# Performance work log

Hardware: AMD Instinct MI355X
Metric: run time of the kernel (lower is better)

Reference implementation:

```python
import math
import jax, jax.numpy as jnp
import numpy as np

B, S, D = 2, 2048, 1024
N_HEADS, D_KV = 16, 64
INNER = N_HEADS * D_KV
NUM_BUCKETS = 32
MAX_DISTANCE = 128


def _relative_position_bucket(relative_position, num_buckets=NUM_BUCKETS, max_distance=MAX_DISTANCE):
    # bidirectional (encoder) variant
    nb = num_buckets // 2
    rel_buckets = (relative_position > 0).astype(jnp.int32) * nb
    rp = jnp.abs(relative_position)
    max_exact = nb // 2
    is_small = rp < max_exact
    rp_safe = jnp.maximum(rp, 1)  # avoid log(0); selected away by where
    rp_if_large = max_exact + (
        jnp.log(rp_safe.astype(jnp.float32) / max_exact)
        / math.log(max_distance / max_exact)
        * (nb - max_exact)
    ).astype(jnp.int32)
    rp_if_large = jnp.minimum(rp_if_large, nb - 1)
    return rel_buckets + jnp.where(is_small, rp, rp_if_large)


def compute_bias(rel_bias, q_len, k_len):
    ctx = jnp.arange(q_len)[:, None]
    mem = jnp.arange(k_len)[None, :]
    buckets = _relative_position_bucket(mem - ctx)  # [q_len, k_len]
    values = rel_bias[buckets]                      # [q_len, k_len, H]
    return jnp.transpose(values, (2, 0, 1))[None]   # [1, H, q_len, k_len]


def setup_inputs() -> dict:
    key = jax.random.key(0)
    ks = jax.random.split(key, 6)
    s = 1.0 / math.sqrt(D)
    return {
        "hidden_states": jax.random.normal(ks[0], (B, S, D), jnp.float32),
        "wq": jax.random.normal(ks[1], (D, INNER), jnp.float32) * s,
        "wk": jax.random.normal(ks[2], (D, INNER), jnp.float32) * s,
        "wv": jax.random.normal(ks[3], (D, INNER), jnp.float32) * s,
        "wo": jax.random.normal(ks[4], (INNER, D), jnp.float32) * s,
        "rel_bias": jax.random.normal(ks[5], (NUM_BUCKETS, N_HEADS), jnp.float32) * 0.1,
    }


def reference(hidden_states, wq, wk, wv, wo, rel_bias):
    b, s, _ = hidden_states.shape

    def shape(x):  # [b, s, inner] -> [b, h, s, d_kv]
        return x.reshape(b, s, N_HEADS, D_KV).transpose(0, 2, 1, 3)

    q = shape(hidden_states @ wq)  # note: T5 has NO 1/sqrt(d) scaling
    k = shape(hidden_states @ wk)
    v = shape(hidden_states @ wv)

    scores = jnp.einsum("bhqd,bhkd->bhqk", q, k)
    position_bias = compute_bias(rel_bias, s, s)
    scores = scores + position_bias
    attn = jax.nn.softmax(scores.astype(jnp.float32), axis=-1).astype(scores.dtype)

    out = jnp.einsum("bhqk,bhkd->bhqd", attn, v)
    out = out.transpose(0, 2, 1, 3).reshape(b, s, INNER)
    return out @ wo
```

## Files before the change

### kernel.cpp

```cpp
#include <hip/hip_runtime.h>
#include <hip/hip_bf16.h>

#define B_ 2
#define S_ 2048
#define D_ 1024
#define H_ 16
#define DKV_ 64
#define INNER_ 1024
#define M_ (B_*S_)

typedef unsigned short ushort_t;
typedef unsigned int u32;
typedef __bf16 bf16x8 __attribute__((ext_vector_type(8)));
typedef __bf16 bf16x4 __attribute__((ext_vector_type(4)));
typedef float f32x4 __attribute__((ext_vector_type(4)));

#define VMCNT0 asm volatile("s_waitcnt vmcnt(0)" ::: "memory")
#define VMCNT4 asm volatile("s_waitcnt vmcnt(4)" ::: "memory")
#define LOG2E 1.4426950408889634f

__device__ __forceinline__ unsigned short f2bf(float f) {
    unsigned int u = __builtin_bit_cast(unsigned int, f);
    unsigned int r = (u + 0x7fffu + ((u >> 16) & 1u)) >> 16;
    return (unsigned short)r;
}

__device__ __forceinline__ void gload16(const ushort_t* g, ushort_t* l) {
    __builtin_amdgcn_global_load_lds(
        (const __attribute__((address_space(1))) u32*)g,
        (__attribute__((address_space(3))) u32*)l, 16, 0, 0);
}

__global__ __launch_bounds__(256) void cvt_bf16(const float* __restrict__ in,
                                                unsigned short* __restrict__ out, int n) {
    int i = (blockIdx.x * 256 + threadIdx.x) * 4;
    if (i < n) {
        float4 v = *(const float4*)&in[i];
        ushort4 o;
        o.x = f2bf(v.x); o.y = f2bf(v.y); o.z = f2bf(v.z); o.w = f2bf(v.w);
        *(ushort4*)&out[i] = o;
    }
}

__global__ __launch_bounds__(256) void transp_bf16(
        const float* __restrict__ s0, const float* __restrict__ s1,
        const float* __restrict__ s2, const float* __restrict__ s3,
        unsigned short* __restrict__ d0, unsigned short* __restrict__ d1,
        unsigned short* __restrict__ d2, unsigned short* __restrict__ d3) {
    const float* srcs[4] = {s0, s1, s2, s3};
    unsigned short* dsts[4] = {d0, d1, d2, d3};
    const float* src = srcs[blockIdx.z];
    unsigned short* dst = dsts[blockIdx.z];
    __shared__ float t[64][65];
    int k0 = blockIdx.y * 64, n0 = blockIdx.x * 64;
    for (int i = threadIdx.x; i < 4096; i += 256) {
        int r = i >> 6, c = i & 63;
        t[r][c] = src[(k0 + r) * 1024 + n0 + c];
    }
    __syncthreads();
    for (int i = threadIdx.x; i < 4096; i += 256) {
        int r = i >> 6, c = i & 63;
        dst[(n0 + r) * 1024 + k0 + c] = f2bf(t[c][r]);
    }
}

__global__ __launch_bounds__(256) void bias_kernel(const float* __restrict__ rb,
                                                   float* __restrict__ btab) {
    int idx = blockIdx.x * 256 + threadIdx.x;
    int h = idx >> 12, pos = idx & 4095;
    int rel = pos - 2048;
    int bb = rel > 0 ? 16 : 0;
    int rp = rel < 0 ? -rel : rel;
    int bucket;
    if (rp < 8) bucket = bb + rp;
    else {
        int v = 8 + (int)(logf((float)rp * 0.125f) / 2.7725887f * 8.0f);
        bucket = bb + (v < 15 ? v : 15);
    }
    btab[idx] = rb[bucket * 16 + h] * LOG2E;
}

__global__ __launch_bounds__(256) void gemm_qkv(const ushort_t* __restrict__ A,
        const ushort_t* __restrict__ WQ, const ushort_t* __restrict__ WK, const ushort_t* __restrict__ WV,
        ushort_t* __restrict__ Qb, ushort_t* __restrict__ Kb, ushort_t* __restrict__ Vtb) {
    __shared__ alignas(16) ushort_t As[128][64];
    __shared__ alignas(16) ushort_t Bs[128][64];
    int tid = threadIdx.x, wid = tid >> 6, lane = tid & 63;
    int linear = blockIdx.x;
    int swz = (linear & 7) * 96 + (linear >> 3);
    int m0 = (swz / 24) * 128;
    int nblk = swz % 24;
    int sel = nblk >> 3;
    const ushort_t* Bt = sel == 0 ? WQ : (sel == 1 ? WK : WV);
    int n0 = (nblk & 7) * 128;
    int lr = lane & 15, lg = lane >> 4;
    int wm = (wid >> 1) * 64, wn = (wid & 1) * 64;
    int srow = tid >> 3, sp = tid & 7;
    int scol = (sp ^ (srow & 7)) * 8;
    int cR0 = (lg ^ (lr & 7)) * 8;
    int cR1 = ((4 + lg) ^ (lr & 7)) * 8;
    const ushort_t* Abase = A + (size_t)m0 * 1024 + scol;
    const ushort_t* Bbase = Bt + (size_t)n0 * 1024 + scol;
    f32x4 acc[4][4] = {};
    for (int kt = 0; kt < 1024; kt += 64) {
        #pragma unroll
        for (int j = 0; j < 4; ++j) {
            int row = j * 32 + srow;
            gload16(Abase + row * 1024 + kt, &As[0][0] + (j * 256 + tid) * 8);
            gload16(Bbase + row * 1024 + kt, &Bs[0][0] + (j * 256 + tid) * 8);
        }
        VMCNT0;
        __syncthreads();
        bf16x8 af[4][2], bfr[4][2];
        #pragma unroll
        for (int t = 0; t < 4; ++t) {
            af[t][0]  = *(const bf16x8*)&As[wm + t * 16 + lr][cR0];
            af[t][1]  = *(const bf16x8*)&As[wm + t * 16 + lr][cR1];
            bfr[t][0] = *(const bf16x8*)&Bs[wn + t * 16 + lr][cR0];
            bfr[t][1] = *(const bf16x8*)&Bs[wn + t * 16 + lr][cR1];
        }
        #pragma unroll
        for (int hh = 0; hh < 2; ++hh)
            #pragma unroll
            for (int i2 = 0; i2 < 4; ++i2)
                #pragma unroll
                for (int j2 = 0; j2 < 4; ++j2)
                    acc[i2][j2] = __builtin_amdgcn_mfma_f32_16x16x32_bf16(af[i2][hh], bfr[j2][hh], acc[i2][j2], 0, 0, 0);
        __syncthreads();
    }
    #pragma unroll
    for (int i2 = 0; i2 < 4; ++i2)
        #pragma unroll
        for (int j2 = 0; j2 < 4; ++j2) {
            int col = n0 + wn + j2 * 16 + lr;
            int hh = col >> 6, d = col & 63;
            if (sel < 2) {
                ushort_t* dst = sel == 0 ? Qb : Kb;
                #pragma unroll
                for (int r = 0; r < 4; ++r) {
                    int row = m0 + wm + i2 * 16 + lg * 4 + r;
                    int b = row >> 11, s = row & 2047;
                    dst[(((size_t)(b * H_ + hh) * S_ + s)) * DKV_ + d] = f2bf(acc[i2][j2][r]);
                }
            } else {
                int row0 = m0 + wm + i2 * 16 + lg * 4;
                int b = row0 >> 11, s0 = row0 & 2047;
                ushort4 sv;
                sv.x = f2bf(acc[i2][j2][0]); sv.y = f2bf(acc[i2][j2][1]);
                sv.z = f2bf(acc[i2][j2][2]); sv.w = f2bf(acc[i2][j2][3]);
                *(ushort4*)&Vtb[((size_t)(b * H_ + hh) * DKV_ + d) * S_ + s0] = sv;
            }
        }
}

__global__ __launch_bounds__(256) void gemm_out(const ushort_t* __restrict__ A,
                                                const ushort_t* __restrict__ Bt,
                                                float* __restrict__ C) {
    __shared__ alignas(16) ushort_t As[64][64];
    __shared__ alignas(16) ushort_t Bs[128][64];
    int tid = threadIdx.x, wid = tid >> 6, lane = tid & 63;
    int linear = blockIdx.x;
    int swz = (linear & 7) * 64 + (linear >> 3);
    int m0 = (swz >> 3) * 64, n0 = (swz & 7) * 128;
    int lr = lane & 15, lg = lane >> 4;
    int wn = wid * 32;
    int srow = tid >> 3, sp = tid & 7;
    int scol = (sp ^ (srow & 7)) * 8;
    int cR0 = (lg ^ (lr & 7)) * 8;
    int cR1 = ((4 + lg) ^ (lr & 7)) * 8;
    const ushort_t* Abase = A + (size_t)m0 * 1024 + scol;
    const ushort_t* Bbase = Bt + (size_t)n0 * 1024 + scol;
    f32x4 acc[4][2] = {};
    for (int kt = 0; kt < 1024; kt += 64) {
        #pragma unroll
        for (int j = 0; j < 2; ++j) {
            int row = j * 32 + srow;
            gload16(Abase + row * 1024 + kt, &As[0][0] + (j * 256 + tid) * 8);
        }
        #pragma unroll
        for (int j = 0; j < 4; ++j) {
            int row = j * 32 + srow;
            gload16(Bbase + row * 1024 + kt, &Bs[0][0] + (j * 256 + tid) * 8);
        }
        VMCNT0;
        __syncthreads();
        bf16x8 af[4][2], bfr[2][2];
        #pragma unroll
        for (int t = 0; t < 4; ++t) {
            af[t][0] = *(const bf16x8*)&As[t * 16 + lr][cR0];
            af[t][1] = *(const bf16x8*)&As[t * 16 + lr][cR1];
        }
        #pragma unroll
        for (int j = 0; j < 2; ++j) {
            bfr[j][0] = *(const bf16x8*)&Bs[wn + j * 16 + lr][cR0];
            bfr[j][1] = *(const bf16x8*)&Bs[wn + j * 16 + lr][cR1];
        }
        #pragma unroll
        for (int hh = 0; hh < 2; ++hh)
            #pragma unroll
            for (int i2 = 0; i2 < 4; ++i2)
                #pragma unroll
                for (int j2 = 0; j2 < 2; ++j2)
                    acc[i2][j2] = __builtin_amdgcn_mfma_f32_16x16x32_bf16(af[i2][hh], bfr[j2][hh], acc[i2][j2], 0, 0, 0);
        __syncthreads();
    }
    #pragma unroll
    for (int i2 = 0; i2 < 4; ++i2)
        #pragma unroll
        for (int j2 = 0; j2 < 2; ++j2)
            #pragma unroll
            for (int r = 0; r < 4; ++r)
                C[(size_t)(m0 + i2 * 16 + lg * 4 + r) * 1024 + n0 + wn + j2 * 16 + lr] = acc[i2][j2][r];
}

__global__ __launch_bounds__(256) void flash_attn(const ushort_t* __restrict__ Q,
                                                  const ushort_t* __restrict__ Kg,
                                                  const ushort_t* __restrict__ Vt,
                                                  const float* __restrict__ bias_tab,
                                                  ushort_t* __restrict__ Out) {
    __shared__ alignas(16) ushort_t Ks[3][64][64];
    __shared__ alignas(16) ushort_t Vs[3][64][64];
    __shared__ alignas(16) ushort_t Ps[4][16][64];
    __shared__ float LbS[2176];
    int tid = threadIdx.x, wid = tid >> 6, lane = tid & 63;
    int linear = blockIdx.x;
    int swz = (linear & 7) * 64 + (linear >> 3);
    int bh = swz >> 4, qblk = swz & 15;
    int h = bh & 15, b = bh >> 4;
    int q0b = qblk * 128;
    int q0w = q0b + wid * 32;
    int lr = lane & 15, lg = lane >> 4;

    {
        const float* bsrc = bias_tab + h * 4096 + 2048 - q0b - 127;
        for (int i = tid; i < 2175; i += 256) LbS[i] = bsrc[i];
    }

    const ushort_t* Qbase = Q + ((size_t)bh * S_ + q0w) * DKV_;
    bf16x8 qA0 = *(const bf16x8*)&Qbase[lr * DKV_ + lg * 8];
    bf16x8 qA1 = *(const bf16x8*)&Qbase[lr * DKV_ + 32 + lg * 8];
    bf16x8 qB0 = *(const bf16x8*)&Qbase[(16 + lr) * DKV_ + lg * 8];
    bf16x8 qB1 = *(const bf16x8*)&Qbase[(16 + lr) * DKV_ + 32 + lg * 8];

    int srow = tid >> 3, sp = tid & 7;
    int kc = (sp ^ (srow & 7)) * 8;
    const ushort_t* Ksrc = Kg + (size_t)bh * S_ * DKV_ + kc;
    const ushort_t* Vsrc = Vt + (size_t)bh * DKV_ * S_ + kc;
    int c0 = (lg ^ (lr & 7)) * 8;
    int c1 = ((4 + lg) ^ (lr & 7)) * 8;
    int pxor = (lr & 7) << 4;

    f32x4 oA[4] = {}, oB[4] = {};
    f32x4 lpA = {}, lpB = {};
    float mA = -INFINITY, mB = -INFINITY;
    const int bbA = 127 - wid * 32 + 4 * lg - lr;
    const int bbB = bbA - 16;

    auto stage = [&](int bi, int kt) {
        ushort_t* kb = &Ks[bi][0][0];
        ushort_t* vb = &Vs[bi][0][0];
        gload16(Ksrc + (size_t)(kt + srow) * 64,      kb + tid * 8);
        gload16(Ksrc + (size_t)(kt + 32 + srow) * 64, kb + 2048 + tid * 8);
        gload16(Vsrc + (size_t)srow * S_ + kt,        vb + tid * 8);
        gload16(Vsrc + (size_t)(32 + srow) * S_ + kt, vb + 2048 + tid * 8);
    };

    stage(0, 0);
    stage(1, 64);
    VMCNT4;
    __syncthreads();
    int cur = 0;
    for (int t = 0; t < 32; ++t) {
        const int kt = t * 64;
        if (t < 30) {
            int nxt = cur + 2; if (nxt >= 3) nxt -= 3;
            stage(nxt, kt + 128);
        }
        f32x4 sA[4] = {}, sB[4] = {};
        #pragma unroll
        for (int nt = 0; nt < 4; ++nt) {
            bf16x8 kf0 = *(const bf16x8*)&Ks[cur][nt * 16 + lr][c0];
            bf16x8 kf1 = *(const bf16x8*)&Ks[cur][nt * 16 + lr][c1];
            sA[nt] = __builtin_amdgcn_mfma_f32_16x16x32_bf16(kf0, qA0, sA[nt], 0, 0, 0);
            sA[nt] = __builtin_amdgcn_mfma_f32_16x16x32_bf16(kf1, qA1, sA[nt], 0, 0, 0);
            sB[nt] = __builtin_amdgcn_mfma_f32_16x16x32_bf16(kf0, qB0, sB[nt], 0, 0, 0);
            sB[nt] = __builtin_amdgcn_mfma_f32_16x16x32_bf16(kf1, qB1, sB[nt], 0, 0, 0);
        }
        char* pbase = (char*)&Ps[wid][lr][0];
        bf16x8 pfA0, pfA1;
        {
            float p[4][4]; float mnt[4];
            const int bi = kt + bbA;
            #pragma unroll
            for (int nt = 0; nt < 4; ++nt) {
                #pragma unroll
                for (int r = 0; r < 4; ++r)
                    p[nt][r] = fmaf(sA[nt][r], LOG2E, LbS[bi + nt * 16 + r]);
                mnt[nt] = fmaxf(fmaxf(p[nt][0], p[nt][1]), fmaxf(p[nt][2], p[nt][3]));
            }
            float mt = fmaxf(fmaxf(mnt[0], mnt[1]), fmaxf(mnt[2], mnt[3]));
            mt = fmaxf(mt, __shfl_xor(mt, 16));
            mt = fmaxf(mt, __shfl_xor(mt, 32));
            if (!__all(mt <= mA + 8.f)) {
                float mnew = fmaxf(mA, mt);
                float sc = __builtin_amdgcn_exp2f(mA - mnew);
                mA = mnew;
                lpA *= sc;
                #pragma unroll
                for (int dt = 0; dt < 4; ++dt) oA[dt] *= sc;
            }
            #pragma unroll
            for (int nt = 0; nt < 4; ++nt) {
                #pragma unroll
                for (int r = 0; r < 4; ++r) {
                    p[nt][r] = __builtin_amdgcn_exp2f(p[nt][r] - mA);
                    lpA[r] += p[nt][r];
                }
                bf16x4 pv;
                pv[0] = (__bf16)p[nt][0]; pv[1] = (__bf16)p[nt][1];
                pv[2] = (__bf16)p[nt][2]; pv[3] = (__bf16)p[nt][3];
                *(bf16x4*)(pbase + ((nt * 32 + lg * 8) ^ pxor)) = pv;
            }
            pfA0 = *(const bf16x8*)(pbase + ((lg * 16) ^ pxor));
            pfA1 = *(const bf16x8*)(pbase + ((64 + lg * 16) ^ pxor));
        }
        bf16x8 pfB0, pfB1;
        {
            float p[4][4]; float mnt[4];
            const int bi = kt + bbB;
            #pragma unroll
            for (int nt = 0; nt < 4; ++nt) {
                #pragma unroll
                for (int r = 0; r < 4; ++r)
                    p[nt][r] = fmaf(sB[nt][r], LOG2E, LbS[bi + nt * 16 + r]);
                mnt[nt] = fmaxf(fmaxf(p[nt][0], p[nt][1]), fmaxf(p[nt][2], p[nt][3]));
            }
            float mt = fmaxf(fmaxf(mnt[0], mnt[1]), fmaxf(mnt[2], mnt[3]));
            mt = fmaxf(mt, __shfl_xor(mt, 16));
            mt = fmaxf(mt, __shfl_xor(mt, 32));
            if (!__all(mt <= mB + 8.f)) {
                float mnew = fmaxf(mB, mt);
                float sc = __builtin_amdgcn_exp2f(mB - mnew);
                mB = mnew;
                lpB *= sc;
                #pragma unroll
                for (int dt = 0; dt < 4; ++dt) oB[dt] *= sc;
            }
            #pragma unroll
            for (int nt = 0; nt < 4; ++nt) {
                #pragma unroll
                for (int r = 0; r < 4; ++r) {
                    p[nt][r] = __builtin_amdgcn_exp2f(p[nt][r] - mB);
                    lpB[r] += p[nt][r];
                }
                bf16x4 pv;
                pv[0] = (__bf16)p[nt][0]; pv[1] = (__bf16)p[nt][1];
                pv[2] = (__bf16)p[nt][2]; pv[3] = (__bf16)p[nt][3];
                *(bf16x4*)(pbase + ((nt * 32 + lg * 8) ^ pxor)) = pv;
            }
            pfB0 = *(const bf16x8*)(pbase + ((lg * 16) ^ pxor));
            pfB1 = *(const bf16x8*)(pbase + ((64 + lg * 16) ^ pxor));
        }
        #pragma unroll
        for (int dt = 0; dt < 4; ++dt) {
            bf16x8 vf0 = *(const bf16x8*)&Vs[cur][dt * 16 + lr][c0];
            bf16x8 vf1 = *(const bf16x8*)&Vs[cur][dt * 16 + lr][c1];
            oA[dt] = __builtin_amdgcn_mfma_f32_16x16x32_bf16(vf0, pfA0, oA[dt], 0, 0, 0);
            oA[dt] = __builtin_amdgcn_mfma_f32_16x16x32_bf16(vf1, pfA1, oA[dt], 0, 0, 0);
            oB[dt] = __builtin_amdgcn_mfma_f32_16x16x32_bf16(vf0, pfB0, oB[dt], 0, 0, 0);
            oB[dt] = __builtin_amdgcn_mfma_f32_16x16x32_bf16(vf1, pfB1, oB[dt], 0, 0, 0);
        }
        if (t < 30) { VMCNT4; } else { VMCNT0; }
        __syncthreads();
        ++cur; if (cur >= 3) cur = 0;
    }
    float lA = (lpA[0] + lpA[1]) + (lpA[2] + lpA[3]);
    lA += __shfl_xor(lA, 16); lA += __shfl_xor(lA, 32);
    float lB = (lpB[0] + lpB[1]) + (lpB[2] + lpB[3]);
    lB += __shfl_xor(lB, 16); lB += __shfl_xor(lB, 32);
    {
        float linv = 1.f / lA;
        char* pbase = (char*)&Ps[wid][lr][0];
        #pragma unroll
        for (int dt = 0; dt < 4; ++dt) {
            bf16x4 ov;
            ov[0] = (__bf16)(oA[dt][0] * linv); ov[1] = (__bf16)(oA[dt][1] * linv);
            ov[2] = (__bf16)(oA[dt][2] * linv); ov[3] = (__bf16)(oA[dt][3] * linv);
            *(bf16x4*)(pbase + ((dt * 32 + lg * 8) ^ pxor)) = ov;
        }
        int row = lane >> 2, seg = lane & 3;
        int rxor = (row & 7) << 4;
        char* rbase = (char*)&Ps[wid][row][0];
        uint4 v0 = *(uint4*)(rbase + ((seg * 32) ^ rxor));
        uint4 v1 = *(uint4*)(rbase + ((seg * 32 + 16) ^ rxor));
        ushort_t* dst = Out + (size_t)(b * S_ + q0w + row) * INNER_ + h * DKV_ + seg * 16;
        *(uint4*)&dst[0] = v0;
        *(uint4*)&dst[8] = v1;
    }
    {
        float linv = 1.f / lB;
        char* pbase = (char*)&Ps[wid][lr][0];
        #pragma unroll
        for (int dt = 0; dt < 4; ++dt) {
            bf16x4 ov;
            ov[0] = (__bf16)(oB[dt][0] * linv); ov[1] = (__bf16)(oB[dt][1] * linv);
            ov[2] = (__bf16)(oB[dt][2] * linv); ov[3] = (__bf16)(oB[dt][3] * linv);
            *(bf16x4*)(pbase + ((dt * 32 + lg * 8) ^ pxor)) = ov;
        }
        int row = lane >> 2, seg = lane & 3;
        int rxor = (row & 7) << 4;
        char* rbase = (char*)&Ps[wid][row][0];
        uint4 v0 = *(uint4*)(rbase + ((seg * 32) ^ rxor));
        uint4 v1 = *(uint4*)(rbase + ((seg * 32 + 16) ^ rxor));
        ushort_t* dst = Out + (size_t)(b * S_ + q0w + 16 + row) * INNER_ + h * DKV_ + seg * 16;
        *(uint4*)&dst[0] = v0;
        *(uint4*)&dst[8] = v1;
    }
}

extern "C" void kernel_launch(void* const* d_in, const int* in_sizes, int n_in,
                              void* d_out, int out_size, void* d_ws, size_t ws_size,
                              hipStream_t stream) {
    const float* hs = (const float*)d_in[0];
    const float* wq = (const float*)d_in[1];
    const float* wk = (const float*)d_in[2];
    const float* wv = (const float*)d_in[3];
    const float* wo = (const float*)d_in[4];
    const float* rb = (const float*)d_in[5];

    char* ws = (char*)d_ws;
    unsigned short* Abf = (unsigned short*)(ws);
    unsigned short* Wqt = (unsigned short*)(ws + (8u  << 20));
    unsigned short* Wkt = (unsigned short*)(ws + (10u << 20));
    unsigned short* Wvt = (unsigned short*)(ws + (12u << 20));
    unsigned short* Wot = (unsigned short*)(ws + (14u << 20));
    unsigned short* Qb  = (unsigned short*)(ws + (16u << 20));
    unsigned short* Kb  = (unsigned short*)(ws + (24u << 20));
    unsigned short* Vtb = (unsigned short*)(ws + (32u << 20));
    unsigned short* AOb = (unsigned short*)(ws + (40u << 20));
    float*          Btab = (float*)(ws + (48u << 20));

    cvt_bf16<<<4096, 256, 0, stream>>>(hs, Abf, M_ * D_);
    transp_bf16<<<dim3(16, 16, 4), 256, 0, stream>>>(wq, wk, wv, wo, Wqt, Wkt, Wvt, Wot);
    bias_kernel<<<256, 256, 0, stream>>>(rb, Btab);

    gemm_qkv<<<768, 256, 0, stream>>>(Abf, Wqt, Wkt, Wvt, Qb, Kb, Vtb);

    flash_attn<<<512, 256, 0, stream>>>(Qb, Kb, Vtb, Btab, AOb);

    gemm_out<<<512, 256, 0, stream>>>(AOb, Wot, (float*)d_out);
}
```

Measured before the change: 137.8 us.

## Fuse prep kernels, double-buffer attention tiles, skip far bias loads, add setprio

```diff
diff --git a/kernel.cpp b/kernel.cpp
--- a/kernel.cpp
+++ b/kernel.cpp
@@ -16,7 +16,6 @@
 typedef float f32x4 __attribute__((ext_vector_type(4)));
 
 #define VMCNT0 asm volatile("s_waitcnt vmcnt(0)" ::: "memory")
-#define VMCNT4 asm volatile("s_waitcnt vmcnt(4)" ::: "memory")
 #define LOG2E 1.4426950408889634f
 
 __device__ __forceinline__ unsigned short f2bf(float f) {
@@ -31,53 +30,57 @@
         (__attribute__((address_space(3))) u32*)l, 16, 0, 0);
 }
 
-__global__ __launch_bounds__(256) void cvt_bf16(const float* __restrict__ in,
-                                                unsigned short* __restrict__ out, int n) {
-    int i = (blockIdx.x * 256 + threadIdx.x) * 4;
-    if (i < n) {
-        float4 v = *(const float4*)&in[i];
+__global__ __launch_bounds__(256) void prep_kernel(
+        const float* __restrict__ hs,
+        const float* __restrict__ s0, const float* __restrict__ s1,
+        const float* __restrict__ s2, const float* __restrict__ s3,
+        const float* __restrict__ rb,
+        unsigned short* __restrict__ Abf,
+        unsigned short* __restrict__ d0, unsigned short* __restrict__ d1,
+        unsigned short* __restrict__ d2, unsigned short* __restrict__ d3,
+        float* __restrict__ btab) {
+    int bid = blockIdx.x, tid = threadIdx.x;
+    if (bid < 4096) {
+        int i = (bid * 256 + tid) * 4;
+        float4 v = *(const float4*)&hs[i];
         ushort4 o;
         o.x = f2bf(v.x); o.y = f2bf(v.y); o.z = f2bf(v.z); o.w = f2bf(v.w);
-        *(ushort4*)&out[i] = o;
-    }
-}
-
-__global__ __launch_bounds__(256) void transp_bf16(
-        const float* __restrict__ s0, const float* __restrict__ s1,
-        const float* __restrict__ s2, const float* __restrict__ s3,
-        unsigned short* __restrict__ d0, unsigned short* __restrict__ d1,
-        unsigned short* __restrict__ d2, unsigned short* __restrict__ d3) {
-    const float* srcs[4] = {s0, s1, s2, s3};
-    unsigned short* dsts[4] = {d0, d1, d2, d3};
-    const float* src = srcs[blockIdx.z];
-    unsigned short* dst = dsts[blockIdx.z];
-    __shared__ float t[64][65];
-    int k0 = blockIdx.y * 64, n0 = blockIdx.x * 64;
-    for (int i = threadIdx.x; i < 4096; i += 256) {
-        int r = i >> 6, c = i & 63;
-        t[r][c] = src[(k0 + r) * 1024 + n0 + c];
-    }
-    __syncthreads();
-    for (int i = threadIdx.x; i < 4096; i += 256) {
-        int r = i >> 6, c = i & 63;
-        dst[(n0 + r) * 1024 + k0 + c] = f2bf(t[c][r]);
-    }
-}
-
-__global__ __launch_bounds__(256) void bias_kernel(const float* __restrict__ rb,
-                                                   float* __restrict__ btab) {
-    int idx = blockIdx.x * 256 + threadIdx.x;
-    int h = idx >> 12, pos = idx & 4095;
-    int rel = pos - 2048;
-    int bb = rel > 0 ? 16 : 0;
-    int rp = rel < 0 ? -rel : rel;
-    int bucket;
-    if (rp < 8) bucket = bb + rp;
-    else {
-        int v = 8 + (int)(logf((float)rp * 0.125f) / 2.7725887f * 8.0f);
-        bucket = bb + (v < 15 ? v : 15);
-    }
-    btab[idx] = rb[bucket * 16 + h] * LOG2E;
+        *(ushort4*)&Abf[i] = o;
+    } else if (bid < 5120) {
+        int t = bid - 4096;
+        int z = t >> 8, rem = t & 255;
+        int k0 = ((rem >> 4) & 15) * 64, n0 = (rem & 15) * 64;
+        const float* srcs[4] = {s0, s1, s2, s3};
+        unsigned short* dsts[4] = {d0, d1, d2, d3};
+        const float* src = srcs[z];
+        unsigned short* dst = dsts[z];
+        __shared__ float tbuf[64][65];
+        for (int i = tid; i < 4096; i += 256) {
+            int r = i >> 6, c = i & 63;
+            tbuf[r][c] = src[(k0 + r) * 1024 + n0 + c];
+        }
+        __syncthreads();
+        for (int i = tid; i < 4096; i += 256) {
+            int r = i >> 6, c = i & 63;
+            dst[(n0 + r) * 1024 + k0 + c] = f2bf(tbuf[c][r]);
+        }
+    } else {
+        #pragma unroll
+        for (int j = 0; j < 4; ++j) {
+            int idx = (bid - 5120) * 1024 + j * 256 + tid;
+            int h = idx >> 12, pos = idx & 4095;
+            int rel = pos - 2048;
+            int bb = rel > 0 ? 16 : 0;
+            int rp = rel < 0 ? -rel : rel;
+            int bucket;
+            if (rp < 8) bucket = bb + rp;
+            else {
+                int v = 8 + (int)(logf((float)rp * 0.125f) / 2.7725887f * 8.0f);
+                bucket = bb + (v < 15 ? v : 15);
+            }
+            btab[idx] = rb[bucket * 16 + h] * LOG2E;
+        }
+    }
 }
 
 __global__ __launch_bounds__(256) void gemm_qkv(const ushort_t* __restrict__ A,
@@ -218,8 +221,8 @@
                                                   const ushort_t* __restrict__ Vt,
                                                   const float* __restrict__ bias_tab,
                                                   ushort_t* __restrict__ Out) {
-    __shared__ alignas(16) ushort_t Ks[3][64][64];
-    __shared__ alignas(16) ushort_t Vs[3][64][64];
+    __shared__ alignas(16) ushort_t Ks[2][64][64];
+    __shared__ alignas(16) ushort_t Vs[2][64][64];
     __shared__ alignas(16) ushort_t Ps[4][16][64];
     __shared__ float LbS[2176];
     int tid = threadIdx.x, wid = tid >> 6, lane = tid & 63;
@@ -235,6 +238,8 @@
         const float* bsrc = bias_tab + h * 4096 + 2048 - q0b - 127;
         for (int i = tid; i < 2175; i += 256) LbS[i] = bsrc[i];
     }
+    float cpos = bias_tab[h * 4096 + 4095];
+    float cneg = bias_tab[h * 4096 + 0];
 
     const ushort_t* Qbase = Q + ((size_t)bh * S_ + q0w) * DKV_;
     bf16x8 qA0 = *(const bf16x8*)&Qbase[lr * DKV_ + lg * 8];
@@ -256,27 +261,29 @@
     const int bbA = 127 - wid * 32 + 4 * lg - lr;
     const int bbB = bbA - 16;
 
-    auto stage = [&](int bi, int kt) {
+    auto stageK = [&](int bi, int kt) {
         ushort_t* kb = &Ks[bi][0][0];
-        ushort_t* vb = &Vs[bi][0][0];
         gload16(Ksrc + (size_t)(kt + srow) * 64,      kb + tid * 8);
         gload16(Ksrc + (size_t)(kt + 32 + srow) * 64, kb + 2048 + tid * 8);
+    };
+    auto stageV = [&](int bi, int kt) {
+        ushort_t* vb = &Vs[bi][0][0];
         gload16(Vsrc + (size_t)srow * S_ + kt,        vb + tid * 8);
         gload16(Vsrc + (size_t)(32 + srow) * S_ + kt, vb + 2048 + tid * 8);
     };
 
-    stage(0, 0);
-    stage(1, 64);
-    VMCNT4;
-    __syncthreads();
-    int cur = 0;
+    stageV(0, 0);
+    stageK(0, 0);
+    asm volatile("s_waitcnt vmcnt(0) lgkmcnt(0)" ::: "memory");
+    __builtin_amdgcn_s_barrier();
+    __builtin_amdgcn_sched_barrier(0);
+
     for (int t = 0; t < 32; ++t) {
         const int kt = t * 64;
-        if (t < 30) {
-            int nxt = cur + 2; if (nxt >= 3) nxt -= 3;
-            stage(nxt, kt + 128);
-        }
+        const int cur = t & 1;
+        if (t < 31) { stageV(cur ^ 1, kt + 64); stageK(cur ^ 1, kt + 64); }
         f32x4 sA[4] = {}, sB[4] = {};
+        __builtin_amdgcn_s_setprio(1);
         #pragma unroll
         for (int nt = 0; nt < 4; ++nt) {
             bf16x8 kf0 = *(const bf16x8*)&Ks[cur][nt * 16 + lr][c0];
@@ -286,16 +293,31 @@
             sB[nt] = __builtin_amdgcn_mfma_f32_16x16x32_bf16(kf0, qB0, sB[nt], 0, 0, 0);
             sB[nt] = __builtin_amdgcn_mfma_f32_16x16x32_bf16(kf1, qB1, sB[nt], 0, 0, 0);
         }
+        __builtin_amdgcn_s_setprio(0);
+        const bool far = (kt >= q0b + 256) || (kt + 64 <= q0b - 128);
+        const float cb = (kt > q0b) ? cpos : cneg;
         char* pbase = (char*)&Ps[wid][lr][0];
         bf16x8 pfA0, pfA1;
         {
+            float bb[4][4];
+            if (far) {
+                #pragma unroll
+                for (int nt = 0; nt < 4; ++nt)
+                    #pragma unroll
+                    for (int r = 0; r < 4; ++r) bb[nt][r] = cb;
+            } else {
+                const int bi = kt + bbA;
+                #pragma unroll
+                for (int nt = 0; nt < 4; ++nt)
+                    #pragma unroll
+                    for (int r = 0; r < 4; ++r) bb[nt][r] = LbS[bi + nt * 16 + r];
+            }
             float p[4][4]; float mnt[4];
-            const int bi = kt + bbA;
             #pragma unroll
             for (int nt = 0; nt < 4; ++nt) {
                 #pragma unroll
                 for (int r = 0; r < 4; ++r)
-                    p[nt][r] = fmaf(sA[nt][r], LOG2E, LbS[bi + nt * 16 + r]);
+                    p[nt][r] = fmaf(sA[nt][r], LOG2E, bb[nt][r]);
                 mnt[nt] = fmaxf(fmaxf(p[nt][0], p[nt][1]), fmaxf(p[nt][2], p[nt][3]));
             }
             float mt = fmaxf(fmaxf(mnt[0], mnt[1]), fmaxf(mnt[2], mnt[3]));
@@ -324,15 +346,36 @@
             pfA0 = *(const bf16x8*)(pbase + ((lg * 16) ^ pxor));
             pfA1 = *(const bf16x8*)(pbase + ((64 + lg * 16) ^ pxor));
         }
+        __builtin_amdgcn_s_setprio(1);
+        #pragma unroll
+        for (int dt = 0; dt < 4; ++dt) {
+            bf16x8 vf0 = *(const bf16x8*)&Vs[cur][dt * 16 + lr][c0];
+            bf16x8 vf1 = *(const bf16x8*)&Vs[cur][dt * 16 + lr][c1];
+            oA[dt] = __builtin_amdgcn_mfma_f32_16x16x32_bf16(vf0, pfA0, oA[dt], 0, 0, 0);
+            oA[dt] = __builtin_amdgcn_mfma_f32_16x16x32_bf16(vf1, pfA1, oA[dt], 0, 0, 0);
+        }
+        __builtin_amdgcn_s_setprio(0);
         bf16x8 pfB0, pfB1;
         {
+            float bb[4][4];
+            if (far) {
+                #pragma unroll
+                for (int nt = 0; nt < 4; ++nt)
+                    #pragma unroll
+                    for (int r = 0; r < 4; ++r) bb[nt][r] = cb;
+            } else {
+                const int bi = kt + bbB;
+                #pragma unroll
+                for (int nt = 0; nt < 4; ++nt)
+                    #pragma unroll
+                    for (int r = 0; r < 4; ++r) bb[nt][r] = LbS[bi + nt * 16 + r];
+            }
             float p[4][4]; float mnt[4];
-            const int bi = kt + bbB;
             #pragma unroll
             for (int nt = 0; nt < 4; ++nt) {
                 #pragma unroll
                 for (int r = 0; r < 4; ++r)
-                    p[nt][r] = fmaf(sB[nt][r], LOG2E, LbS[bi + nt * 16 + r]);
+                    p[nt][r] = fmaf(sB[nt][r], LOG2E, bb[nt][r]);
                 mnt[nt] = fmaxf(fmaxf(p[nt][0], p[nt][1]), fmaxf(p[nt][2], p[nt][3]));
             }
             float mt = fmaxf(fmaxf(mnt[0], mnt[1]), fmaxf(mnt[2], mnt[3]));
@@ -361,18 +404,20 @@
             pfB0 = *(const bf16x8*)(pbase + ((lg * 16) ^ pxor));
             pfB1 = *(const bf16x8*)(pbase + ((64 + lg * 16) ^ pxor));
         }
+        __builtin_amdgcn_s_setprio(1);
         #pragma unroll
         for (int dt = 0; dt < 4; ++dt) {
             bf16x8 vf0 = *(const bf16x8*)&Vs[cur][dt * 16 + lr][c0];
             bf16x8 vf1 = *(const bf16x8*)&Vs[cur][dt * 16 + lr][c1];
-            oA[dt] = __builtin_amdgcn_mfma_f32_16x16x32_bf16(vf0, pfA0, oA[dt], 0, 0, 0);
-            oA[dt] = __builtin_amdgcn_mfma_f32_16x16x32_bf16(vf1, pfA1, oA[dt], 0, 0, 0);
             oB[dt] = __builtin_amdgcn_mfma_f32_16x16x32_bf16(vf0, pfB0, oB[dt], 0, 0, 0);
             oB[dt] = __builtin_amdgcn_mfma_f32_16x16x32_bf16(vf1, pfB1, oB[dt], 0, 0, 0);
         }
-        if (t < 30) { VMCNT4; } else { VMCNT0; }
-        __syncthreads();
-        ++cur; if (cur >= 3) cur = 0;
+        __builtin_amdgcn_s_setprio(0);
+        if (t < 31) {
+            asm volatile("s_waitcnt vmcnt(0)" ::: "memory");
+            __builtin_amdgcn_s_barrier();
+            __builtin_amdgcn_sched_barrier(0);
+        }
     }
     float lA = (lpA[0] + lpA[1]) + (lpA[2] + lpA[3]);
     lA += __shfl_xor(lA, 16); lA += __shfl_xor(lA, 32);
@@ -440,9 +485,8 @@
     unsigned short* AOb = (unsigned short*)(ws + (40u << 20));
     float*          Btab = (float*)(ws + (48u << 20));
 
-    cvt_bf16<<<4096, 256, 0, stream>>>(hs, Abf, M_ * D_);
-    transp_bf16<<<dim3(16, 16, 4), 256, 0, stream>>>(wq, wk, wv, wo, Wqt, Wkt, Wvt, Wot);
-    bias_kernel<<<256, 256, 0, stream>>>(rb, Btab);
+    prep_kernel<<<5184, 256, 0, stream>>>(hs, wq, wk, wv, wo, rb,
+                                          Abf, Wqt, Wkt, Wvt, Wot, Btab);
 
     gemm_qkv<<<768, 256, 0, stream>>>(Abf, Wqt, Wkt, Wvt, Qb, Kb, Vtb);
 
```

After: 133.9 us. 2.8% less time.
